# Optimization experiments

Measured on AMD Instinct MI355X. Metric: run time of the kernel, lower is better.

Reference implementation:

```python
import jax, jax.numpy as jnp
import numpy as np

E = 1024
H = 16
D = E // H
B = 4
NQ = 4096
NK = 4096
LN_EPS = 1e-5


def setup_inputs() -> dict:
    key = jax.random.key(0)
    ks = jax.random.split(key, 16)
    s = 1.0 / np.sqrt(E)
    return {
        "query_embed": jax.random.normal(ks[0], (B, NQ, E), jnp.float32),
        "key_embed": jax.random.normal(ks[1], (B, NK, E), jnp.float32),
        "value": jax.random.normal(ks[2], (B, NK, E), jnp.float32),
        "Wq": jax.random.normal(ks[3], (E, E), jnp.float32) * s,
        "bq": jax.random.normal(ks[4], (E,), jnp.float32) * s,
        "Wk": jax.random.normal(ks[5], (E, E), jnp.float32) * s,
        "bk": jax.random.normal(ks[6], (E,), jnp.float32) * s,
        "Wv": jax.random.normal(ks[7], (E, E), jnp.float32) * s,
        "bv": jax.random.normal(ks[8], (E,), jnp.float32) * s,
        "Wo": jax.random.normal(ks[9], (E, E), jnp.float32) * s,
        "bo": jax.random.normal(ks[10], (E,), jnp.float32) * s,
        "gq": jnp.ones((E,), jnp.float32),
        "betaq": jnp.zeros((E,), jnp.float32),
        "gk": jnp.ones((E,), jnp.float32),
        "betak": jnp.zeros((E,), jnp.float32),
    }


def _layernorm(x, g, b):
    mu = jnp.mean(x, axis=-1, keepdims=True)
    var = jnp.mean(jnp.square(x - mu), axis=-1, keepdims=True)
    return (x - mu) * jax.lax.rsqrt(var + LN_EPS) * g + b


def reference(query_embed, key_embed, value, Wq, bq, Wk, bk, Wv, bv, Wo, bo,
              gq, betaq, gk, betak):
    Bq, Nq, _ = query_embed.shape
    _, Nk, _ = key_embed.shape
    # projections (torch Linear: x @ W.T + b) + LayerNorm
    q = _layernorm(query_embed @ Wq.T + bq, gq, betaq).reshape(Bq, Nq, H, D)
    k = _layernorm(key_embed @ Wk.T + bk, gk, betak).reshape(Bq, Nk, H, D)
    v = (value @ Wv.T + bv).reshape(Bq, Nk, H, D)
    # elu + 1 feature map
    q = jax.nn.elu(q) + 1.0  # [B, Nq, H, D]
    k = jax.nn.elu(k) + 1.0  # [B, Nk, H, D]
    # linear attention: O(N*d^2)
    kv_sum = jnp.einsum('bnhd,bnhe->bhde', k, v)        # [B, H, D, D]
    k_sum = jnp.sum(k, axis=1)                          # [B, H, D]
    num = jnp.einsum('bqhd,bhde->bqhe', q, kv_sum)      # [B, Nq, H, D]
    den = jnp.einsum('bqhd,bhd->bqh', q, k_sum)[..., None] + 1e-8
    out = (num / den).reshape(Bq, Nq, H * D)
    return out @ Wo.T + bo
```

## Files before the change

kernel.cpp:

```cpp
#include <hip/hip_runtime.h>
#include <hip/hip_bf16.h>

#define EDIM 1024
#define HHEADS 16
#define DHEAD 64
#define BB 4
#define NSEQ 4096
#define NTOK 16384
#define KVSPLIT 16

typedef unsigned short u16;
using frag8 = __attribute__((ext_vector_type(8))) short;
using facc4 = __attribute__((ext_vector_type(4))) float;

__device__ __forceinline__ float b2f(u16 u) {
  union { unsigned int i; float f; } c; c.i = ((unsigned int)u) << 16; return c.f;
}
__device__ __forceinline__ u16 f2b(float f) {
  __hip_bfloat16 h = __float2bfloat16(f);
  union { __hip_bfloat16 h; u16 u; } c; c.h = h; return c.u;
}
__device__ __forceinline__ void gl2lds16(const void* g, void* l) {
  __builtin_amdgcn_global_load_lds(
      (const __attribute__((address_space(1))) unsigned int*)g,
      (__attribute__((address_space(3))) unsigned int*)l, 16, 0, 0);
}

__global__ void detect_dtype(const u16* __restrict__ src, unsigned* __restrict__ flag) {
  const int lane = threadIdx.x;
  const unsigned u = src[(size_t)lane * 200000];
  const unsigned e = (u >> 7) & 0xFF;
  const bool inl = (u == 0) || (e >= 100 && e <= 135);
  const unsigned long long m = __ballot(inl);
  if (lane == 0) flag[0] = (__popcll(m) >= 32) ? 1u : 0u;
}

__global__ __launch_bounds__(256) void cvt_bf16(
    const void* __restrict__ src, u16* __restrict__ dst, int n,
    const unsigned* __restrict__ flag) {
  if (flag[0] == 1) return;
  const int i0 = (blockIdx.x * 256 + threadIdx.x) * 8;
  if (i0 >= n) return;
  const float4 a = ((const float4*)src)[i0 >> 2];
  const float4 b = ((const float4*)src)[(i0 >> 2) + 1];
  ushort4 lo, hi;
  lo.x = f2b(a.x); lo.y = f2b(a.y); lo.z = f2b(a.z); lo.w = f2b(a.w);
  hi.x = f2b(b.x); hi.y = f2b(b.y); hi.z = f2b(b.z); hi.w = f2b(b.w);
  ((ushort4*)dst)[i0 >> 2] = lo;
  ((ushort4*)dst)[(i0 >> 2) + 1] = hi;
}

struct Ptr8 { const void* s[8]; u16* d[8]; };
__global__ __launch_bounds__(256) void cvt8(Ptr8 p, const unsigned* __restrict__ flag) {
  const int t = blockIdx.x * 256 + threadIdx.x;
  const int v = t >> 7;
  const int i0 = (t & 127) * 8;
  const void* s = p.s[v];
  u16* d = p.d[v];
  ushort4 lo, hi;
  if (flag[0] == 0) {
    const float4 a = ((const float4*)s)[i0 >> 2];
    const float4 b = ((const float4*)s)[(i0 >> 2) + 1];
    lo.x = f2b(a.x); lo.y = f2b(a.y); lo.z = f2b(a.z); lo.w = f2b(a.w);
    hi.x = f2b(b.x); hi.y = f2b(b.y); hi.z = f2b(b.z); hi.w = f2b(b.w);
  } else {
    lo = ((const ushort4*)s)[i0 >> 2];
    hi = ((const ushort4*)s)[(i0 >> 2) + 1];
  }
  ((ushort4*)d)[i0 >> 2] = lo;
  ((ushort4*)d)[(i0 >> 2) + 1] = hi;
}

__global__ __launch_bounds__(256, 2) void gemm_bias(
    const void* __restrict__ Araw, const u16* __restrict__ Acvt,
    const void* __restrict__ Wraw, const u16* __restrict__ Wcvt,
    const u16* __restrict__ bias, u16* __restrict__ C,
    const unsigned* __restrict__ flag, int outMode)
{
  __shared__ __align__(16) u16 As[128 * 32];
  __shared__ __align__(16) u16 Bs[128 * 32];
  const int tid  = threadIdx.x;
  const int lane = tid & 63;
  const int w    = tid >> 6;
  const int wm   = w >> 1, wn = w & 1;
  const int rowBase = blockIdx.x * 128;
  const int colBase = blockIdx.y * 128;

  const bool bfw = (flag[0] == 1);
  const u16* A = bfw ? (const u16*)Araw : Acvt;
  const u16* W = bfw ? (const u16*)Wraw : Wcvt;

  facc4 acc[4][4];
#pragma unroll
  for (int i = 0; i < 4; ++i)
#pragma unroll
    for (int j = 0; j < 4; ++j) acc[i][j] = (facc4){0.f, 0.f, 0.f, 0.f};

  const int sRow = w * 32 + (lane >> 2);
  const int sCol = (lane & 3) * 8;
  const u16* Ag = A + (size_t)(rowBase + sRow) * EDIM + sCol;
  const u16* Wg = W + (size_t)(colBase + sRow) * EDIM + sCol;
  u16* AsB = As + w * 1024;
  u16* BsB = Bs + w * 1024;

  const int fr = lane & 15;
  const int kq = (lane >> 4) * 8;

  for (int k0 = 0; k0 < EDIM; k0 += 32) {
    gl2lds16(Ag + k0,            AsB);
    gl2lds16(Ag + k0 + 16*EDIM,  AsB + 512);
    gl2lds16(Wg + k0,            BsB);
    gl2lds16(Wg + k0 + 16*EDIM,  BsB + 512);
    __syncthreads();
    frag8 af[4], bf[4];
#pragma unroll
    for (int i = 0; i < 4; ++i)
      af[i] = *(const frag8*)(As + (wm * 64 + i * 16 + fr) * 32 + kq);
#pragma unroll
    for (int j = 0; j < 4; ++j)
      bf[j] = *(const frag8*)(Bs + (wn * 64 + j * 16 + fr) * 32 + kq);
#pragma unroll
    for (int i = 0; i < 4; ++i)
#pragma unroll
      for (int j = 0; j < 4; ++j)
        acc[i][j] = __builtin_amdgcn_mfma_f32_16x16x32_bf16(af[i], bf[j], acc[i][j], 0, 0, 0);
    __syncthreads();
  }

  const bool f32out = (outMode == 1) && !bfw;
  float* Cf = (float*)C;
  float bvv[4];
#pragma unroll
  for (int j = 0; j < 4; ++j)
    bvv[j] = b2f(bias[colBase + wn * 64 + j * 16 + fr]);
#pragma unroll
  for (int i = 0; i < 4; ++i) {
#pragma unroll
    for (int r = 0; r < 4; ++r) {
      const int row = rowBase + wm * 64 + i * 16 + (lane >> 4) * 4 + r;
      const size_t ro = (size_t)row * EDIM + colBase + wn * 64 + fr;
#pragma unroll
      for (int j = 0; j < 4; ++j) {
        const float val = acc[i][j][r] + bvv[j];
        if (f32out) Cf[ro + j * 16] = val;
        else        C[ro + j * 16]  = f2b(val);
      }
    }
  }
}

__global__ __launch_bounds__(256) void ln_elu(
    const u16* __restrict__ X, const u16* __restrict__ g,
    const u16* __restrict__ beta, u16* __restrict__ Y)
{
  __shared__ float wsum[4], wsq[4];
  const int row = blockIdx.x, tid = threadIdx.x;
  const ushort4 xu = ((const ushort4*)(X + (size_t)row * EDIM))[tid];
  float x[4] = { b2f(xu.x), b2f(xu.y), b2f(xu.z), b2f(xu.w) };
  float s  = x[0] + x[1] + x[2] + x[3];
  float ss = x[0]*x[0] + x[1]*x[1] + x[2]*x[2] + x[3]*x[3];
#pragma unroll
  for (int off = 32; off > 0; off >>= 1) {
    s  += __shfl_down(s,  off, 64);
    ss += __shfl_down(ss, off, 64);
  }
  if ((tid & 63) == 0) { wsum[tid >> 6] = s; wsq[tid >> 6] = ss; }
  __syncthreads();
  const float S  = wsum[0] + wsum[1] + wsum[2] + wsum[3];
  const float SS = wsq[0] + wsq[1] + wsq[2] + wsq[3];
  const float mu  = S * (1.0f / EDIM);
  const float var = SS * (1.0f / EDIM) - mu * mu;
  const float rs  = rsqrtf(var + 1e-5f);
  const ushort4 gu = ((const ushort4*)g)[tid];
  const ushort4 bu = ((const ushort4*)beta)[tid];
  float gg[4] = { b2f(gu.x), b2f(gu.y), b2f(gu.z), b2f(gu.w) };
  float bb[4] = { b2f(bu.x), b2f(bu.y), b2f(bu.z), b2f(bu.w) };
  ushort4 out;
  u16 o[4];
#pragma unroll
  for (int c = 0; c < 4; ++c) {
    float y = (x[c] - mu) * rs * gg[c] + bb[c];
    y = (y > 0.f) ? (y + 1.f) : __expf(y);
    o[c] = f2b(y);
  }
  out.x = o[0]; out.y = o[1]; out.z = o[2]; out.w = o[3];
  ((ushort4*)(Y + (size_t)row * EDIM))[tid] = out;
}

__global__ __launch_bounds__(256) void kv_partial(
    const u16* __restrict__ Km, const u16* __restrict__ V,
    float* __restrict__ partials, float* __restrict__ kspart)
{
  __shared__ __align__(16) u16 smem[2 * 64 * 130];
  u16 (*kT)[130] = (u16(*)[130])smem;
  u16 (*vT)[130] = (u16(*)[130])(smem + 64 * 130);
  float* red = (float*)smem;
  float* ksr = ((float*)smem) + 4352;

  const int split = blockIdx.x, h = blockIdx.y, b = blockIdx.z;
  const int bh = b * HHEADS + h;
  const int tid = threadIdx.x, lane = tid & 63, w = tid >> 6;
  const size_t base = (size_t)b * NSEQ * EDIM + h * DHEAD;
  const int nbase = split * (NSEQ / KVSPLIT);

  float ksacc[8] = {0, 0, 0, 0, 0, 0, 0, 0};
  facc4 acc[4][4];
#pragma unroll
  for (int i = 0; i < 4; ++i)
#pragma unroll
    for (int j = 0; j < 4; ++j) acc[i][j] = (facc4){0.f, 0.f, 0.f, 0.f};

  const int e0 = (tid & 7) * 8;
  const int nl0 = tid >> 3;
  const int fr = lane & 15;
  const int quad = lane >> 4;

  for (int c = 0; c < 2; ++c) {
    const int nchunk = nbase + c * 128;
#pragma unroll
    for (int rep = 0; rep < 4; ++rep) {
      const int n = rep * 32 + nl0;
      const uint4 kd = *(const uint4*)(Km + base + (size_t)(nchunk + n) * EDIM + e0);
      const uint4 vd = *(const uint4*)(V  + base + (size_t)(nchunk + n) * EDIM + e0);
      const u16* pk = (const u16*)&kd;
      const u16* pv = (const u16*)&vd;
#pragma unroll
      for (int ii = 0; ii < 8; ++ii) {
        kT[e0 + ii][n] = pk[ii];
        ksacc[ii] += b2f(pk[ii]);
        vT[e0 + ii][n] = pv[ii];
      }
    }
    __syncthreads();
    const int kq2 = w * 32 + quad * 8;
    frag8 af[4], bf[4];
#pragma unroll
    for (int i = 0; i < 4; ++i) af[i] = *(const frag8*)&kT[i * 16 + fr][kq2];
#pragma unroll
    for (int j = 0; j < 4; ++j) bf[j] = *(const frag8*)&vT[j * 16 + fr][kq2];
#pragma unroll
    for (int i = 0; i < 4; ++i)
#pragma unroll
      for (int j = 0; j < 4; ++j)
        acc[i][j] = __builtin_amdgcn_mfma_f32_16x16x32_bf16(af[i], bf[j], acc[i][j], 0, 0, 0);
    __syncthreads();
  }

  for (int p = 0; p < 4; ++p) {
    const int j = (w + p) & 3;
#pragma unroll
    for (int i = 0; i < 4; ++i)
#pragma unroll
      for (int r = 0; r < 4; ++r) {
        const int d = i * 16 + quad * 4 + r;
        const int e = j * 16 + fr;
        if (p == 0) red[d * 68 + e] = acc[i][j][r];
        else        red[d * 68 + e] += acc[i][j][r];
      }
    __syncthreads();
  }

  const size_t pbase = ((size_t)bh * KVSPLIT + split) * 4096;
#pragma unroll
  for (int ii = 0; ii < 16; ++ii) {
    const int idx = tid + ii * 256;
    partials[pbase + idx] = red[(idx >> 6) * 68 + (idx & 63)];
  }

#pragma unroll
  for (int ii = 0; ii < 8; ++ii) {
    ksacc[ii] += __shfl_down(ksacc[ii], 32, 64);
    ksacc[ii] += __shfl_down(ksacc[ii], 16, 64);
    ksacc[ii] += __shfl_down(ksacc[ii], 8, 64);
  }
  if (lane < 8) {
#pragma unroll
    for (int ii = 0; ii < 8; ++ii) ksr[w * 64 + lane * 8 + ii] = ksacc[ii];
  }
  __syncthreads();
  if (tid < 64)
    kspart[((size_t)bh * KVSPLIT + split) * 64 + tid] =
        ksr[tid] + ksr[64 + tid] + ksr[128 + tid] + ksr[192 + tid];
}

__global__ __launch_bounds__(256) void kv_reduce(
    const float* __restrict__ partials, const float* __restrict__ kspart,
    float* __restrict__ KV, float* __restrict__ Ks)
{
  const int qt = blockIdx.x;
  const int bh = blockIdx.y;
  const int tid = threadIdx.x;
#pragma unroll
  for (int ii = 0; ii < 4; ++ii) {
    const int idx = qt * 1024 + ii * 256 + tid;
    float s = 0.f;
#pragma unroll
    for (int sp = 0; sp < KVSPLIT; ++sp)
      s += partials[((size_t)bh * KVSPLIT + sp) * 4096 + idx];
    KV[(size_t)bh * 4096 + idx] = s;
  }
  if (qt == 0 && tid < 64) {
    float s = 0.f;
#pragma unroll
    for (int sp = 0; sp < KVSPLIT; ++sp)
      s += kspart[((size_t)bh * KVSPLIT + sp) * 64 + tid];
    Ks[bh * 64 + tid] = s;
  }
}

__global__ __launch_bounds__(256) void attn_nd(
    const u16* __restrict__ Q, const float* __restrict__ KV,
    const float* __restrict__ Ks, u16* __restrict__ O)
{
  __shared__ __align__(16) u16 kvT[64][72];
  __shared__ float ks_s[64];
  __shared__ float den_s[4][16];
  const int qt = blockIdx.x, h = blockIdx.y, b = blockIdx.z;
  const int bh = b * HHEADS + h;
  const int tid = threadIdx.x, lane = tid & 63, w = tid >> 6;
  const float* kvp = KV + (size_t)bh * 4096;
#pragma unroll
  for (int ii = 0; ii < 16; ++ii) {
    const int idx = tid + ii * 256;
    kvT[idx & 63][idx >> 6] = f2b(kvp[idx]);
  }
  if (tid < 64) ks_s[tid] = Ks[bh * 64 + tid];
  __syncthreads();

  const int fr = lane & 15;
  const int q8 = (lane >> 4) * 8;
  const u16* qp = Q + (size_t)(b * NSEQ + qt * 64 + w * 16 + fr) * EDIM + h * DHEAD;
  const frag8 a0 = *(const frag8*)(qp + q8);
  const frag8 a1 = *(const frag8*)(qp + 32 + q8);

  const u16* a0u = (const u16*)&a0;
  const u16* a1u = (const u16*)&a1;
  float den = 0.f;
#pragma unroll
  for (int j = 0; j < 8; ++j)
    den += b2f(a0u[j]) * ks_s[q8 + j] + b2f(a1u[j]) * ks_s[32 + q8 + j];
  den += __shfl_xor(den, 16, 64);
  den += __shfl_xor(den, 32, 64);
  if (lane < 16) den_s[w][lane] = den + 1e-8f;

  facc4 acc[4];
#pragma unroll
  for (int j = 0; j < 4; ++j) acc[j] = (facc4){0.f, 0.f, 0.f, 0.f};
#pragma unroll
  for (int j = 0; j < 4; ++j) {
    const frag8 b0 = *(const frag8*)&kvT[j * 16 + fr][q8];
    const frag8 b1 = *(const frag8*)&kvT[j * 16 + fr][32 + q8];
    acc[j] = __builtin_amdgcn_mfma_f32_16x16x32_bf16(a0, b0, acc[j], 0, 0, 0);
    acc[j] = __builtin_amdgcn_mfma_f32_16x16x32_bf16(a1, b1, acc[j], 0, 0, 0);
  }
  __syncthreads();
#pragma unroll
  for (int r = 0; r < 4; ++r) {
    const int rq = (lane >> 4) * 4 + r;
    const float dv = den_s[w][rq];
    const size_t orow = (size_t)(b * NSEQ + qt * 64 + w * 16 + rq) * EDIM + h * DHEAD;
#pragma unroll
    for (int j = 0; j < 4; ++j)
      O[orow + j * 16 + fr] = f2b(acc[j][r] / dv);
  }
}

extern "C" void kernel_launch(void* const* d_in, const int* in_sizes, int n_in,
                              void* d_out, int out_size, void* d_ws, size_t ws_size,
                              hipStream_t stream) {
  char* ws = (char*)d_ws;
  const size_t EH = (size_t)NTOK * EDIM;
  unsigned* flag = (unsigned*)ws;
  u16* Wqb  = (u16*)(ws + 1024);
  u16* Wkb  = Wqb + EDIM * EDIM;
  u16* Wvb  = Wkb + EDIM * EDIM;
  u16* Wob  = Wvb + EDIM * EDIM;
  u16* bqb  = Wob + EDIM * EDIM;
  u16* bkb  = bqb + 1024;
  u16* bvb  = bkb + 1024;
  u16* bob  = bvb + 1024;
  u16* gqb  = bob + 1024;
  u16* bEqb = gqb + 1024;
  u16* gkb  = bEqb + 1024;
  u16* bEkb = gkb + 1024;
  u16* Xin  = bEkb + 1024;
  u16* preQ = Xin + EH;
  u16* preK = preQ + EH;
  u16* vbuf = preK + EH;
  float* partials = (float*)(vbuf + EH);
  float* kspart   = partials + (size_t)64 * KVSPLIT * 4096;
  float* kvbuf    = kspart + (size_t)64 * KVSPLIT * 64;
  float* ksbuf    = kvbuf + (size_t)64 * 4096;

  const dim3 gg(NTOK / 128, EDIM / 128), tb(256);
  const int NW = EDIM * EDIM;

  detect_dtype<<<1, 64, 0, stream>>>((const u16*)d_in[0], flag);
  cvt_bf16<<<NW / 2048, 256, 0, stream>>>(d_in[3], Wqb, NW, flag);
  cvt_bf16<<<NW / 2048, 256, 0, stream>>>(d_in[5], Wkb, NW, flag);
  cvt_bf16<<<NW / 2048, 256, 0, stream>>>(d_in[7], Wvb, NW, flag);
  cvt_bf16<<<NW / 2048, 256, 0, stream>>>(d_in[9], Wob, NW, flag);
  Ptr8 p8;
  p8.s[0] = d_in[4];  p8.s[1] = d_in[6];  p8.s[2] = d_in[8];  p8.s[3] = d_in[10];
  p8.s[4] = d_in[11]; p8.s[5] = d_in[12]; p8.s[6] = d_in[13]; p8.s[7] = d_in[14];
  p8.d[0] = bqb; p8.d[1] = bkb; p8.d[2] = bvb; p8.d[3] = bob;
  p8.d[4] = gqb; p8.d[5] = bEqb; p8.d[6] = gkb; p8.d[7] = bEkb;
  cvt8<<<4, 256, 0, stream>>>(p8, flag);

  cvt_bf16<<<EH / 2048, 256, 0, stream>>>(d_in[0], Xin, (int)EH, flag);
  gemm_bias<<<gg, tb, 0, stream>>>(d_in[0], Xin, d_in[3], Wqb, bqb, preQ, flag, 0);
  cvt_bf16<<<EH / 2048, 256, 0, stream>>>(d_in[1], Xin, (int)EH, flag);
  gemm_bias<<<gg, tb, 0, stream>>>(d_in[1], Xin, d_in[5], Wkb, bkb, preK, flag, 0);
  cvt_bf16<<<EH / 2048, 256, 0, stream>>>(d_in[2], Xin, (int)EH, flag);
  gemm_bias<<<gg, tb, 0, stream>>>(d_in[2], Xin, d_in[7], Wvb, bvb, vbuf, flag, 0);

  ln_elu<<<NTOK, 256, 0, stream>>>(preQ, gqb, bEqb, preQ);
  ln_elu<<<NTOK, 256, 0, stream>>>(preK, gkb, bEkb, preK);

  kv_partial<<<dim3(KVSPLIT, HHEADS, BB), tb, 0, stream>>>(preK, vbuf, partials, kspart);
  kv_reduce<<<dim3(4, 64), tb, 0, stream>>>(partials, kspart, kvbuf, ksbuf);
  attn_nd<<<dim3(NSEQ / 64, HHEADS, BB), tb, 0, stream>>>(preQ, kvbuf, ksbuf, Xin);
  gemm_bias<<<gg, tb, 0, stream>>>(Xin, Xin, d_in[9], Wob, bob, (u16*)d_out, flag, 1);
}
```

Before: 542.7 us.

## Fuse fp32-to-bf16 input conversion into GEMM loads and merge small kernels

The standalone conversion passes over the three 16M-element activation inputs are removed. The projection GEMMs now read fp32 activations directly and convert them while staging into LDS, with K per iteration doubled to 64 across two LDS halves. All weight and vector conversions are merged into one launch, and the Q and K LayerNorm+ELU passes into one. This saves a write and reread of each activation in bf16 and several launches. In exchange, the A operand is now loaded synchronously through registers instead of with the async global-to-LDS path, and the loop uses more LDS.

```diff
diff --git a/kernel.cpp b/kernel.cpp
--- a/kernel.cpp
+++ b/kernel.cpp
@@ -35,50 +35,42 @@
   if (lane == 0) flag[0] = (__popcll(m) >= 32) ? 1u : 0u;
 }
 
-__global__ __launch_bounds__(256) void cvt_bf16(
-    const void* __restrict__ src, u16* __restrict__ dst, int n,
-    const unsigned* __restrict__ flag) {
+struct WCvtArgs { const void* s[12]; u16* d[12]; };
+__global__ __launch_bounds__(256) void wcvt(WCvtArgs p, const unsigned* __restrict__ flag) {
   if (flag[0] == 1) return;
-  const int i0 = (blockIdx.x * 256 + threadIdx.x) * 8;
-  if (i0 >= n) return;
-  const float4 a = ((const float4*)src)[i0 >> 2];
-  const float4 b = ((const float4*)src)[(i0 >> 2) + 1];
-  ushort4 lo, hi;
-  lo.x = f2b(a.x); lo.y = f2b(a.y); lo.z = f2b(a.z); lo.w = f2b(a.w);
-  hi.x = f2b(b.x); hi.y = f2b(b.y); hi.z = f2b(b.z); hi.w = f2b(b.w);
-  ((ushort4*)dst)[i0 >> 2] = lo;
-  ((ushort4*)dst)[(i0 >> 2) + 1] = hi;
-}
-
-struct Ptr8 { const void* s[8]; u16* d[8]; };
-__global__ __launch_bounds__(256) void cvt8(Ptr8 p, const unsigned* __restrict__ flag) {
-  const int t = blockIdx.x * 256 + threadIdx.x;
-  const int v = t >> 7;
-  const int i0 = (t & 127) * 8;
-  const void* s = p.s[v];
-  u16* d = p.d[v];
-  ushort4 lo, hi;
-  if (flag[0] == 0) {
-    const float4 a = ((const float4*)s)[i0 >> 2];
-    const float4 b = ((const float4*)s)[(i0 >> 2) + 1];
-    lo.x = f2b(a.x); lo.y = f2b(a.y); lo.z = f2b(a.z); lo.w = f2b(a.w);
-    hi.x = f2b(b.x); hi.y = f2b(b.y); hi.z = f2b(b.z); hi.w = f2b(b.w);
+  const float* src;
+  u16* dst;
+  size_t idx;
+  if (blockIdx.x < 2048) {
+    const int wsel = blockIdx.x >> 9;
+    idx = (size_t)(((blockIdx.x & 511) * 256 + threadIdx.x)) * 8;
+    src = (const float*)p.s[wsel];
+    dst = p.d[wsel];
   } else {
-    lo = ((const ushort4*)s)[i0 >> 2];
-    hi = ((const ushort4*)s)[(i0 >> 2) + 1];
-  }
-  ((ushort4*)d)[i0 >> 2] = lo;
-  ((ushort4*)d)[(i0 >> 2) + 1] = hi;
+    const int t2 = (blockIdx.x - 2048) * 256 + threadIdx.x;
+    const int vsel = 4 + (t2 >> 7);
+    idx = (size_t)(t2 & 127) * 8;
+    src = (const float*)p.s[vsel];
+    dst = p.d[vsel];
+  }
+  const float4 a = *(const float4*)(src + idx);
+  const float4 b = *(const float4*)(src + idx + 4);
+  union { u16 us[8]; uint4 v; } pk;
+  pk.us[0] = f2b(a.x); pk.us[1] = f2b(a.y); pk.us[2] = f2b(a.z); pk.us[3] = f2b(a.w);
+  pk.us[4] = f2b(b.x); pk.us[5] = f2b(b.y); pk.us[6] = f2b(b.z); pk.us[7] = f2b(b.w);
+  *(uint4*)(dst + idx) = pk.v;
 }
 
 __global__ __launch_bounds__(256, 2) void gemm_bias(
-    const void* __restrict__ Araw, const u16* __restrict__ Acvt,
-    const void* __restrict__ Wraw, const u16* __restrict__ Wcvt,
-    const u16* __restrict__ bias, u16* __restrict__ C,
-    const unsigned* __restrict__ flag, int outMode)
+    const void* __restrict__ Araw, const void* __restrict__ Wraw,
+    const u16* __restrict__ Wcvt, const void* __restrict__ biasRaw,
+    const u16* __restrict__ biasCvt, u16* __restrict__ C,
+    const unsigned* __restrict__ flag, int aMode, int outMode)
 {
-  __shared__ __align__(16) u16 As[128 * 32];
-  __shared__ __align__(16) u16 Bs[128 * 32];
+  __shared__ __align__(16) u16 As0[4096];
+  __shared__ __align__(16) u16 As1[4096];
+  __shared__ __align__(16) u16 Bs0[4096];
+  __shared__ __align__(16) u16 Bs1[4096];
   const int tid  = threadIdx.x;
   const int lane = tid & 63;
   const int w    = tid >> 6;
@@ -87,8 +79,9 @@
   const int colBase = blockIdx.y * 128;
 
   const bool bfw = (flag[0] == 1);
-  const u16* A = bfw ? (const u16*)Araw : Acvt;
-  const u16* W = bfw ? (const u16*)Wraw : Wcvt;
+  const u16* W    = bfw ? (const u16*)Wraw    : Wcvt;
+  const u16* bias = bfw ? (const u16*)biasRaw : biasCvt;
+  const bool aBf  = bfw || (aMode == 0);
 
   facc4 acc[4][4];
 #pragma unroll
@@ -98,33 +91,88 @@
 
   const int sRow = w * 32 + (lane >> 2);
   const int sCol = (lane & 3) * 8;
-  const u16* Ag = A + (size_t)(rowBase + sRow) * EDIM + sCol;
   const u16* Wg = W + (size_t)(colBase + sRow) * EDIM + sCol;
-  u16* AsB = As + w * 1024;
-  u16* BsB = Bs + w * 1024;
+  u16* AsB0 = As0 + w * 1024;
+  u16* AsB1 = As1 + w * 1024;
+  u16* BsB0 = Bs0 + w * 1024;
+  u16* BsB1 = Bs1 + w * 1024;
 
   const int fr = lane & 15;
   const int kq = (lane >> 4) * 8;
 
-  for (int k0 = 0; k0 < EDIM; k0 += 32) {
-    gl2lds16(Ag + k0,            AsB);
-    gl2lds16(Ag + k0 + 16*EDIM,  AsB + 512);
-    gl2lds16(Wg + k0,            BsB);
-    gl2lds16(Wg + k0 + 16*EDIM,  BsB + 512);
-    __syncthreads();
-    frag8 af[4], bf[4];
-#pragma unroll
-    for (int i = 0; i < 4; ++i)
-      af[i] = *(const frag8*)(As + (wm * 64 + i * 16 + fr) * 32 + kq);
-#pragma unroll
-    for (int j = 0; j < 4; ++j)
-      bf[j] = *(const frag8*)(Bs + (wn * 64 + j * 16 + fr) * 32 + kq);
-#pragma unroll
-    for (int i = 0; i < 4; ++i)
-#pragma unroll
-      for (int j = 0; j < 4; ++j)
-        acc[i][j] = __builtin_amdgcn_mfma_f32_16x16x32_bf16(af[i], bf[j], acc[i][j], 0, 0, 0);
-    __syncthreads();
+  if (aBf) {
+    const u16* Ag = (const u16*)Araw + (size_t)(rowBase + sRow) * EDIM + sCol;
+    for (int k0 = 0; k0 < EDIM; k0 += 64) {
+      gl2lds16(Ag + k0,                 AsB0);
+      gl2lds16(Ag + k0 + 16 * EDIM,      AsB0 + 512);
+      gl2lds16(Ag + k0 + 32,             AsB1);
+      gl2lds16(Ag + k0 + 32 + 16 * EDIM, AsB1 + 512);
+      gl2lds16(Wg + k0,                 BsB0);
+      gl2lds16(Wg + k0 + 16 * EDIM,      BsB0 + 512);
+      gl2lds16(Wg + k0 + 32,             BsB1);
+      gl2lds16(Wg + k0 + 32 + 16 * EDIM, BsB1 + 512);
+      __syncthreads();
+#pragma unroll
+      for (int s = 0; s < 2; ++s) {
+        const u16* Ah = s ? As1 : As0;
+        const u16* Bh = s ? Bs1 : Bs0;
+        frag8 af[4], bf[4];
+#pragma unroll
+        for (int i = 0; i < 4; ++i)
+          af[i] = *(const frag8*)(Ah + (wm * 64 + i * 16 + fr) * 32 + kq);
+#pragma unroll
+        for (int j = 0; j < 4; ++j)
+          bf[j] = *(const frag8*)(Bh + (wn * 64 + j * 16 + fr) * 32 + kq);
+#pragma unroll
+        for (int i = 0; i < 4; ++i)
+#pragma unroll
+          for (int j = 0; j < 4; ++j)
+            acc[i][j] = __builtin_amdgcn_mfma_f32_16x16x32_bf16(af[i], bf[j], acc[i][j], 0, 0, 0);
+      }
+      __syncthreads();
+    }
+  } else {
+    const float* Af = (const float*)Araw;
+    const int frow = w * 32 + (lane >> 3);
+    const int fcol = (lane & 7) * 8;
+    u16* dhalf = (fcol < 32) ? As0 : As1;
+    const int dcol = fcol & 31;
+    for (int k0 = 0; k0 < EDIM; k0 += 64) {
+#pragma unroll
+      for (int g = 0; g < 4; ++g) {
+        const int r = frow + g * 8;
+        const float* src = Af + (size_t)(rowBase + r) * EDIM + k0 + fcol;
+        const float4 x0 = *(const float4*)src;
+        const float4 x1 = *(const float4*)(src + 4);
+        union { u16 us[8]; uint4 v; } pk;
+        pk.us[0] = f2b(x0.x); pk.us[1] = f2b(x0.y); pk.us[2] = f2b(x0.z); pk.us[3] = f2b(x0.w);
+        pk.us[4] = f2b(x1.x); pk.us[5] = f2b(x1.y); pk.us[6] = f2b(x1.z); pk.us[7] = f2b(x1.w);
+        *(uint4*)(dhalf + (size_t)r * 32 + dcol) = pk.v;
+      }
+      gl2lds16(Wg + k0,                 BsB0);
+      gl2lds16(Wg + k0 + 16 * EDIM,      BsB0 + 512);
+      gl2lds16(Wg + k0 + 32,             BsB1);
+      gl2lds16(Wg + k0 + 32 + 16 * EDIM, BsB1 + 512);
+      __syncthreads();
+#pragma unroll
+      for (int s = 0; s < 2; ++s) {
+        const u16* Ah = s ? As1 : As0;
+        const u16* Bh = s ? Bs1 : Bs0;
+        frag8 af[4], bf[4];
+#pragma unroll
+        for (int i = 0; i < 4; ++i)
+          af[i] = *(const frag8*)(Ah + (wm * 64 + i * 16 + fr) * 32 + kq);
+#pragma unroll
+        for (int j = 0; j < 4; ++j)
+          bf[j] = *(const frag8*)(Bh + (wn * 64 + j * 16 + fr) * 32 + kq);
+#pragma unroll
+        for (int i = 0; i < 4; ++i)
+#pragma unroll
+          for (int j = 0; j < 4; ++j)
+            acc[i][j] = __builtin_amdgcn_mfma_f32_16x16x32_bf16(af[i], bf[j], acc[i][j], 0, 0, 0);
+      }
+      __syncthreads();
+    }
   }
 
   const bool f32out = (outMode == 1) && !bfw;
@@ -149,12 +197,24 @@
   }
 }
 
-__global__ __launch_bounds__(256) void ln_elu(
-    const u16* __restrict__ X, const u16* __restrict__ g,
-    const u16* __restrict__ beta, u16* __restrict__ Y)
+__global__ __launch_bounds__(256) void ln_elu2(
+    u16* __restrict__ Xq, u16* __restrict__ Xk,
+    const void* __restrict__ gqRaw, const u16* __restrict__ gqCvt,
+    const void* __restrict__ bqRaw, const u16* __restrict__ bqCvt,
+    const void* __restrict__ gkRaw, const u16* __restrict__ gkCvt,
+    const void* __restrict__ bkRaw, const u16* __restrict__ bkCvt,
+    const unsigned* __restrict__ flag)
 {
   __shared__ float wsum[4], wsq[4];
-  const int row = blockIdx.x, tid = threadIdx.x;
+  const bool bfw = (flag[0] == 1);
+  const bool isK = blockIdx.x >= NTOK;
+  const int row  = isK ? (blockIdx.x - NTOK) : blockIdx.x;
+  u16* X = isK ? Xk : Xq;
+  const u16* g    = isK ? (bfw ? (const u16*)gkRaw : gkCvt)
+                        : (bfw ? (const u16*)gqRaw : gqCvt);
+  const u16* beta = isK ? (bfw ? (const u16*)bkRaw : bkCvt)
+                        : (bfw ? (const u16*)bqRaw : bqCvt);
+  const int tid = threadIdx.x;
   const ushort4 xu = ((const ushort4*)(X + (size_t)row * EDIM))[tid];
   float x[4] = { b2f(xu.x), b2f(xu.y), b2f(xu.z), b2f(xu.w) };
   float s  = x[0] + x[1] + x[2] + x[3];
@@ -184,7 +244,7 @@
     o[c] = f2b(y);
   }
   out.x = o[0]; out.y = o[1]; out.z = o[2]; out.w = o[3];
-  ((ushort4*)(Y + (size_t)row * EDIM))[tid] = out;
+  ((ushort4*)(X + (size_t)row * EDIM))[tid] = out;
 }
 
 __global__ __launch_bounds__(256) void kv_partial(
@@ -393,32 +453,28 @@
   float* ksbuf    = kvbuf + (size_t)64 * 4096;
 
   const dim3 gg(NTOK / 128, EDIM / 128), tb(256);
-  const int NW = EDIM * EDIM;
 
   detect_dtype<<<1, 64, 0, stream>>>((const u16*)d_in[0], flag);
-  cvt_bf16<<<NW / 2048, 256, 0, stream>>>(d_in[3], Wqb, NW, flag);
-  cvt_bf16<<<NW / 2048, 256, 0, stream>>>(d_in[5], Wkb, NW, flag);
-  cvt_bf16<<<NW / 2048, 256, 0, stream>>>(d_in[7], Wvb, NW, flag);
-  cvt_bf16<<<NW / 2048, 256, 0, stream>>>(d_in[9], Wob, NW, flag);
-  Ptr8 p8;
-  p8.s[0] = d_in[4];  p8.s[1] = d_in[6];  p8.s[2] = d_in[8];  p8.s[3] = d_in[10];
-  p8.s[4] = d_in[11]; p8.s[5] = d_in[12]; p8.s[6] = d_in[13]; p8.s[7] = d_in[14];
-  p8.d[0] = bqb; p8.d[1] = bkb; p8.d[2] = bvb; p8.d[3] = bob;
-  p8.d[4] = gqb; p8.d[5] = bEqb; p8.d[6] = gkb; p8.d[7] = bEkb;
-  cvt8<<<4, 256, 0, stream>>>(p8, flag);
-
-  cvt_bf16<<<EH / 2048, 256, 0, stream>>>(d_in[0], Xin, (int)EH, flag);
-  gemm_bias<<<gg, tb, 0, stream>>>(d_in[0], Xin, d_in[3], Wqb, bqb, preQ, flag, 0);
-  cvt_bf16<<<EH / 2048, 256, 0, stream>>>(d_in[1], Xin, (int)EH, flag);
-  gemm_bias<<<gg, tb, 0, stream>>>(d_in[1], Xin, d_in[5], Wkb, bkb, preK, flag, 0);
-  cvt_bf16<<<EH / 2048, 256, 0, stream>>>(d_in[2], Xin, (int)EH, flag);
-  gemm_bias<<<gg, tb, 0, stream>>>(d_in[2], Xin, d_in[7], Wvb, bvb, vbuf, flag, 0);
-
-  ln_elu<<<NTOK, 256, 0, stream>>>(preQ, gqb, bEqb, preQ);
-  ln_elu<<<NTOK, 256, 0, stream>>>(preK, gkb, bEkb, preK);
+
+  WCvtArgs wa;
+  wa.s[0] = d_in[3];  wa.s[1] = d_in[5];  wa.s[2] = d_in[7];  wa.s[3] = d_in[9];
+  wa.s[4] = d_in[4];  wa.s[5] = d_in[6];  wa.s[6] = d_in[8];  wa.s[7] = d_in[10];
+  wa.s[8] = d_in[11]; wa.s[9] = d_in[12]; wa.s[10] = d_in[13]; wa.s[11] = d_in[14];
+  wa.d[0] = Wqb; wa.d[1] = Wkb; wa.d[2] = Wvb; wa.d[3] = Wob;
+  wa.d[4] = bqb; wa.d[5] = bkb; wa.d[6] = bvb; wa.d[7] = bob;
+  wa.d[8] = gqb; wa.d[9] = bEqb; wa.d[10] = gkb; wa.d[11] = bEkb;
+  wcvt<<<2052, 256, 0, stream>>>(wa, flag);
+
+  gemm_bias<<<gg, tb, 0, stream>>>(d_in[0], d_in[3], Wqb, d_in[4],  bqb, preQ, flag, 1, 0);
+  gemm_bias<<<gg, tb, 0, stream>>>(d_in[1], d_in[5], Wkb, d_in[6],  bkb, preK, flag, 1, 0);
+  gemm_bias<<<gg, tb, 0, stream>>>(d_in[2], d_in[7], Wvb, d_in[8],  bvb, vbuf, flag, 1, 0);
+
+  ln_elu2<<<2 * NTOK, 256, 0, stream>>>(preQ, preK,
+      d_in[11], gqb, d_in[12], bEqb, d_in[13], gkb, d_in[14], bEkb, flag);
 
   kv_partial<<<dim3(KVSPLIT, HHEADS, BB), tb, 0, stream>>>(preK, vbuf, partials, kspart);
   kv_reduce<<<dim3(4, 64), tb, 0, stream>>>(partials, kspart, kvbuf, ksbuf);
   attn_nd<<<dim3(NSEQ / 64, HHEADS, BB), tb, 0, stream>>>(preQ, kvbuf, ksbuf, Xin);
-  gemm_bias<<<gg, tb, 0, stream>>>(Xin, Xin, d_in[9], Wob, bob, (u16*)d_out, flag, 1);
-}
+
+  gemm_bias<<<gg, tb, 0, stream>>>(Xin, d_in[9], Wob, d_in[10], bob, (u16*)d_out, flag, 0, 1);
+}
```

Result: slower. 629.4 us (+16.0%).
